# Kernel tuning notes

Measured on AMD Instinct MI355X. Metric: run time of the kernel, lower is better.

Reference implementation:

```python
import jax, jax.numpy as jnp
import numpy as np

N = 8192          # num nodes
T = 8             # num node types (== num_bases, full basis)
H = 4             # attention heads
IN = 64           # in_feat
OUT = 64          # out_feat


def setup_inputs() -> dict:
    key = jax.random.key(0)
    ks = jax.random.split(key, 9)
    return {
        "agg_msg": jax.random.normal(ks[0], (N, H * IN), dtype=jnp.float32),
        "h": jax.random.normal(ks[1], (N, OUT), dtype=jnp.float32),
        "node_type": jax.random.randint(ks[2], (N,), 0, T),
        "W_att": jax.random.normal(ks[3], (T, H * IN, IN), dtype=jnp.float32) * 0.05,
        "b_att": jax.random.normal(ks[4], (T, OUT), dtype=jnp.float32) * 0.05,
        "W_in": jax.random.normal(ks[5], (T, IN, 3 * OUT), dtype=jnp.float32) * 0.05,
        "W_hid": jax.random.normal(ks[6], (T, OUT, 3 * OUT), dtype=jnp.float32) * 0.05,
        "b_in": jax.random.normal(ks[7], (T, 3 * OUT), dtype=jnp.float32) * 0.05,
        "b_hid": jax.random.normal(ks[8], (T, 3 * OUT), dtype=jnp.float32) * 0.05,
    }


def reference(agg_msg, h, node_type, W_att, b_att, W_in, W_hid, b_in, b_hid):
    # activation on aggregated message (F.relu)
    x = jax.nn.relu(agg_msg)                                 # [N, H*IN]
    # --- attention-head aggregation: per-node-type weight gather + bmm ---
    Wa = W_att[node_type]                                    # [N, H*IN, IN]  (irregular gather)
    x = jnp.einsum('nd,ndo->no', x, Wa) + b_att[node_type]   # [N, IN]
    x = jax.nn.relu(x)
    # --- GRU-style gated update with per-node-type weights ---
    gi = jnp.einsum('ni,nio->no', x, W_in[node_type]) + b_in[node_type]    # [N, 3*OUT]
    gh = jnp.einsum('nk,nko->no', h, W_hid[node_type]) + b_hid[node_type]  # [N, 3*OUT]
    i_r, i_z, i_n = jnp.split(gi, 3, axis=-1)
    h_r, h_z, h_n = jnp.split(gh, 3, axis=-1)
    r = jax.nn.sigmoid(i_r + h_r)
    z = jax.nn.sigmoid(i_z + h_z)
    n = jnp.tanh(i_n + r * h_n)
    h_new = (1.0 - z) * n + z * h                            # [N, OUT]
    return h_new
```

## Files before the change

kernel.cpp:

```cpp
#include <hip/hip_runtime.h>

#define N_NODES 8192
#define T_TYPES 8
#define HIN 256
#define OUTF 64
#define G3 192
#define BM 32
#define MAXBLK 264
#define SCAT_BLKS 32

typedef __attribute__((ext_vector_type(8))) __bf16 bf16x8;
typedef __attribute__((ext_vector_type(4))) float f32x4;

#define WS_CURS 0
#define WS_PERM 256
#define WS_WAT  (256 + 262144)
#define WS_WIT  (WS_WAT + 262144)
#define WS_WHT  (WS_WIT + 196608)
#define WS_CNT  (WS_WHT + 196608)

#define L_XS  0
#define L_WAS 16384
#define L_WIS 49152
#define L_WHS 73728
#define L_YS  98304
#define L_HS  102400
#define L_HF  106496
#define L_IDX 114688
#define L_TOT 114816

#define GLD_LDS16(g, l) __builtin_amdgcn_global_load_lds( \
    (const __attribute__((address_space(1))) void*)(g),   \
    (__attribute__((address_space(3))) void*)(l), 16, 0, 0)

__device__ __forceinline__ unsigned short f2bf(float f) {
    unsigned u = __float_as_uint(f);
    return (unsigned short)((u + 0x7FFFu + ((u >> 16) & 1u)) >> 16);
}
__device__ __forceinline__ int pack2bf(float a, float b) {
    return (int)f2bf(a) | ((int)f2bf(b) << 16);
}

__global__ __launch_bounds__(256) void prep_and_count(
    const float* __restrict__ W_att, const float* __restrict__ W_in,
    const float* __restrict__ W_hid, const int* __restrict__ nt,
    int* __restrict__ counts,
    unsigned short* __restrict__ waT, unsigned short* __restrict__ wiT,
    unsigned short* __restrict__ whT)
{
    __shared__ float Lf[64][68];
    __shared__ int hist[8];
    const int tid = threadIdx.x;
    const int b = blockIdx.x;

    if (b >= 80) {
        int j = b - 80;
        if (tid < 8) hist[tid] = 0;
        __syncthreads();
        int t = nt[j * 256 + tid];
        atomicAdd(&hist[t], 1);
        __syncthreads();
        if (tid < 8) counts[j * 8 + tid] = hist[tid];
        return;
    }

    const float* src;
    unsigned short* dstBase;
    int srcStride, rowBytes, colBase, rBase;

    if (b < 32) {
        int t = b >> 2, kt = b & 3;
        src = W_att + (((size_t)t * 256 + kt * 64) << 6);
        srcStride = 64;
        dstBase = waT + (size_t)t * 16384;
        rowBytes = 512; colBase = kt * 128; rBase = 0;
    } else {
        int j = b - 32;
        int isWh = (j >= 24); if (isWh) j -= 24;
        int t = j / 3, nt2 = j - t * 3;
        src = (isWh ? W_hid : W_in) + (size_t)t * 64 * 192 + nt2 * 64;
        srcStride = 192;
        dstBase = (isWh ? whT : wiT) + (size_t)t * 12288;
        rowBytes = 128; colBase = 0; rBase = nt2 * 64;
    }

    #pragma unroll
    for (int e = 0; e < 4; ++e) {
        int f = e * 256 + tid;
        int kk = f >> 4, c = (f & 15) << 2;
        float4 v = *(const float4*)(src + kk * srcStride + c);
        Lf[kk][c] = v.x; Lf[kk][c + 1] = v.y; Lf[kk][c + 2] = v.z; Lf[kk][c + 3] = v.w;
    }
    __syncthreads();

    #pragma unroll
    for (int e = 0; e < 2; ++e) {
        int q = e * 256 + tid;
        int ko8 = q >> 6, rl = q & 63;
        int r = rBase + rl;
        unsigned short tmp[8];
        #pragma unroll
        for (int j2 = 0; j2 < 8; ++j2)
            tmp[j2] = f2bf(Lf[ko8 * 8 + j2][rl]);
        int4 wv;
        wv.x = (int)tmp[0] | ((int)tmp[1] << 16);
        wv.y = (int)tmp[2] | ((int)tmp[3] << 16);
        wv.z = (int)tmp[4] | ((int)tmp[5] << 16);
        wv.w = (int)tmp[6] | ((int)tmp[7] << 16);
        int B = r * rowBytes + colBase + ((ko8 << 4) ^ ((r & 7) << 4));
        *(int4*)((char*)dstBase + B) = wv;
    }
}

__global__ __launch_bounds__(256) void scatter_pass(
    const int* __restrict__ nt, const int* __restrict__ counts,
    int* __restrict__ cursors, int* __restrict__ perm)
{
    __shared__ int tbl[SCAT_BLKS * 8];
    __shared__ int cur[8];
    const int tid = threadIdx.x;
    const int j = blockIdx.x;

    tbl[tid & 255] = counts[tid & 255];
    __syncthreads();
    if (tid < 8) {
        int base = 0, tot = 0;
        #pragma unroll
        for (int b = 0; b < SCAT_BLKS; ++b) {
            int c = tbl[b * 8 + tid];
            if (b < j) base += c;
            tot += c;
        }
        cur[tid] = base;
        if (j == 0) cursors[tid] = tot;
    }
    __syncthreads();
    int i = j * 256 + tid;
    int t = nt[i];
    int pos = atomicAdd(&cur[t], 1);
    perm[t * N_NODES + pos] = i;
}

__global__ __launch_bounds__(256) void fused_rgnn(
    const float* __restrict__ agg, const float* __restrict__ h,
    const int* __restrict__ cursors, const int* __restrict__ perm,
    const unsigned short* __restrict__ waT, const unsigned short* __restrict__ wiT,
    const unsigned short* __restrict__ whT,
    const float* __restrict__ b_att, const float* __restrict__ b_in,
    const float* __restrict__ b_hid, float* __restrict__ out)
{
    __shared__ __align__(16) char smem[L_TOT];
    char* sm = smem;

    const int tid = threadIdx.x;
    const int b = blockIdx.x;

    const int4 c0 = *(const int4*)cursors;
    const int4 c1 = *(const int4*)(cursors + 4);
    const int cntArr[8] = {c0.x, c0.y, c0.z, c0.w, c1.x, c1.y, c1.z, c1.w};
    int t = -1, chunk = 0, cnt = 0, acc = 0;
    #pragma unroll
    for (int tt = 0; tt < T_TYPES; ++tt) {
        int nc = (cntArr[tt] + BM - 1) >> 5;
        if (t < 0 && b < acc + nc) { t = tt; chunk = b - acc; cnt = cntArr[tt]; }
        acc += nc;
    }
    if (t < 0) return;
    const int m0 = chunk * BM;
    const int mcnt = min(BM, cnt - m0);

    const int lane = tid & 63;
    const int w = tid >> 6;
    const int lr = lane & 15;
    const int lk = lane >> 4;
    const int col = (w << 4) + lr;
    const int swzA = (lr & 7) << 4;

    const float ba  = b_att[(t << 6) + col];
    const float bir = b_in [t * G3 + col];
    const float biz = b_in [t * G3 + 64 + col];
    const float bnn = b_in [t * G3 + 128 + col];
    const float bhr = b_hid[t * G3 + col];
    const float bhz = b_hid[t * G3 + 64 + col];
    const float bhn = b_hid[t * G3 + 128 + col];

    const int nb = tid >> 5;
    const int kx = (tid & 31) << 3;
    int xg[4];
    #pragma unroll
    for (int s = 0; s < 4; ++s) {
        int node = nb + (s << 3);
        xg[s] = (node < mcnt) ? perm[t * N_NODES + m0 + node] : -1;
    }
    const int nh = tid >> 3;
    const int kh = (tid & 7) << 3;
    int hg = (nh < mcnt) ? perm[t * N_NODES + m0 + nh] : -1;

    float4 xv[4][2];
    #pragma unroll
    for (int s = 0; s < 4; ++s) {
        if (xg[s] >= 0) {
            const float* p = agg + (size_t)xg[s] * HIN + kx;
            xv[s][0] = *(const float4*)p;
            xv[s][1] = *(const float4*)(p + 4);
        } else {
            xv[s][0] = make_float4(0.f, 0.f, 0.f, 0.f);
            xv[s][1] = make_float4(0.f, 0.f, 0.f, 0.f);
        }
    }
    float4 hv0, hv1;
    if (hg >= 0) {
        const float* p = h + (size_t)hg * OUTF + kh;
        hv0 = *(const float4*)p;
        hv1 = *(const float4*)(p + 4);
    } else {
        hv0 = make_float4(0.f, 0.f, 0.f, 0.f);
        hv1 = make_float4(0.f, 0.f, 0.f, 0.f);
    }

    {
        const char* was = (const char*)(waT + (size_t)t * 16384);
        const char* wis = (const char*)(wiT + (size_t)t * 12288);
        const char* whs = (const char*)(whT + (size_t)t * 12288);
        #pragma unroll
        for (int r = 0; r < 8; ++r) {
            int c = (r << 2) + w;
            GLD_LDS16(was + (c << 10) + (lane << 4), sm + L_WAS + (c << 10));
        }
        #pragma unroll
        for (int r = 0; r < 6; ++r) {
            int c = (r << 2) + w;
            GLD_LDS16(wis + (c << 10) + (lane << 4), sm + L_WIS + (c << 10));
            GLD_LDS16(whs + (c << 10) + (lane << 4), sm + L_WHS + (c << 10));
        }
    }

    #pragma unroll
    for (int s = 0; s < 4; ++s) {
        int node = nb + (s << 3);
        float4 a = xv[s][0], bq = xv[s][1];
        int4 wv;
        wv.x = pack2bf(fmaxf(a.x, 0.f), fmaxf(a.y, 0.f));
        wv.y = pack2bf(fmaxf(a.z, 0.f), fmaxf(a.w, 0.f));
        wv.z = pack2bf(fmaxf(bq.x, 0.f), fmaxf(bq.y, 0.f));
        wv.w = pack2bf(fmaxf(bq.z, 0.f), fmaxf(bq.w, 0.f));
        *(int4*)(sm + L_XS + (node << 9) + (((kx << 1)) ^ ((node & 7) << 4))) = wv;
    }
    {
        *(float4*)(sm + L_HF + (nh << 8) + (kh << 2)) = hv0;
        *(float4*)(sm + L_HF + (nh << 8) + (kh << 2) + 16) = hv1;
        int4 wv;
        wv.x = pack2bf(hv0.x, hv0.y);
        wv.y = pack2bf(hv0.z, hv0.w);
        wv.z = pack2bf(hv1.x, hv1.y);
        wv.w = pack2bf(hv1.z, hv1.w);
        *(int4*)(sm + L_HS + (nh << 7) + ((kh << 1) ^ ((nh & 7) << 4))) = wv;
        if ((tid & 7) == 0) ((int*)(sm + L_IDX))[nh] = hg;
    }
    __syncthreads();

    f32x4 acc0 = {0.f, 0.f, 0.f, 0.f}, acc1 = {0.f, 0.f, 0.f, 0.f};
    #pragma unroll
    for (int ks = 0; ks < 8; ++ks) {
        int koffB = (ks << 6) + (lk << 4);
        int off = koffB ^ swzA;
        bf16x8 bb = *(const bf16x8*)(sm + L_WAS + (((w << 4) + lr) << 9) + off);
        bf16x8 a0 = *(const bf16x8*)(sm + L_XS + (lr << 9) + off);
        bf16x8 a1 = *(const bf16x8*)(sm + L_XS + ((16 + lr) << 9) + off);
        acc0 = __builtin_amdgcn_mfma_f32_16x16x32_bf16(a0, bb, acc0, 0, 0, 0);
        acc1 = __builtin_amdgcn_mfma_f32_16x16x32_bf16(a1, bb, acc1, 0, 0, 0);
    }
    #pragma unroll
    for (int m = 0; m < 2; ++m) {
        #pragma unroll
        for (int r = 0; r < 4; ++r) {
            int row = (m << 4) + (lk << 2) + r;
            float y = fmaxf((m ? acc1[r] : acc0[r]) + ba, 0.f);
            *(unsigned short*)(sm + L_YS + (row << 7) +
                               (((col << 1)) ^ ((row & 7) << 4))) = f2bf(y);
        }
    }
    __syncthreads();

    f32x4 gi[2][3], gh[2][3];
    #pragma unroll
    for (int m = 0; m < 2; ++m)
        #pragma unroll
        for (int g = 0; g < 3; ++g) {
            gi[m][g] = (f32x4){0.f, 0.f, 0.f, 0.f};
            gh[m][g] = (f32x4){0.f, 0.f, 0.f, 0.f};
        }
    #pragma unroll
    for (int ks = 0; ks < 2; ++ks) {
        int off = ((ks << 6) + (lk << 4)) ^ swzA;
        bf16x8 ay0 = *(const bf16x8*)(sm + L_YS + (lr << 7) + off);
        bf16x8 ay1 = *(const bf16x8*)(sm + L_YS + ((16 + lr) << 7) + off);
        bf16x8 ah0 = *(const bf16x8*)(sm + L_HS + (lr << 7) + off);
        bf16x8 ah1 = *(const bf16x8*)(sm + L_HS + ((16 + lr) << 7) + off);
        #pragma unroll
        for (int g = 0; g < 3; ++g) {
            int brow = (g << 6) + col;
            bf16x8 bi = *(const bf16x8*)(sm + L_WIS + (brow << 7) + off);
            bf16x8 bh = *(const bf16x8*)(sm + L_WHS + (brow << 7) + off);
            gi[0][g] = __builtin_amdgcn_mfma_f32_16x16x32_bf16(ay0, bi, gi[0][g], 0, 0, 0);
            gi[1][g] = __builtin_amdgcn_mfma_f32_16x16x32_bf16(ay1, bi, gi[1][g], 0, 0, 0);
            gh[0][g] = __builtin_amdgcn_mfma_f32_16x16x32_bf16(ah0, bh, gh[0][g], 0, 0, 0);
            gh[1][g] = __builtin_amdgcn_mfma_f32_16x16x32_bf16(ah1, bh, gh[1][g], 0, 0, 0);
        }
    }

    const int* idxp = (const int*)(sm + L_IDX);
    #pragma unroll
    for (int m = 0; m < 2; ++m) {
        #pragma unroll
        for (int r = 0; r < 4; ++r) {
            int node = (m << 4) + (lk << 2) + r;
            if (node < mcnt) {
                float rv = gi[m][0][r] + bir + gh[m][0][r] + bhr;
                float rg = 1.f / (1.f + __expf(-rv));
                float zv = gi[m][1][r] + biz + gh[m][1][r] + bhz;
                float zg = 1.f / (1.f + __expf(-zv));
                float ng = tanhf(gi[m][2][r] + bnn + rg * (gh[m][2][r] + bhn));
                float hold = *(const float*)(sm + L_HF + (node << 8) + (col << 2));
                out[(size_t)idxp[node] * OUTF + col] = (1.f - zg) * ng + zg * hold;
            }
        }
    }
}

extern "C" void kernel_launch(void* const* d_in, const int* in_sizes, int n_in,
                              void* d_out, int out_size, void* d_ws, size_t ws_size,
                              hipStream_t stream) {
    const float* agg   = (const float*)d_in[0];
    const float* h     = (const float*)d_in[1];
    const int*   ntype = (const int*)d_in[2];
    const float* W_att = (const float*)d_in[3];
    const float* b_att = (const float*)d_in[4];
    const float* W_in  = (const float*)d_in[5];
    const float* W_hid = (const float*)d_in[6];
    const float* b_in  = (const float*)d_in[7];
    const float* b_hid = (const float*)d_in[8];
    float* out = (float*)d_out;

    char* ws = (char*)d_ws;
    int* cursors = (int*)(ws + WS_CURS);
    int* perm = (int*)(ws + WS_PERM);
    unsigned short* waT = (unsigned short*)(ws + WS_WAT);
    unsigned short* wiT = (unsigned short*)(ws + WS_WIT);
    unsigned short* whT = (unsigned short*)(ws + WS_WHT);
    int* counts = (int*)(ws + WS_CNT);

    prep_and_count<<<112, 256, 0, stream>>>(W_att, W_in, W_hid, ntype, counts, waT, wiT, whT);
    scatter_pass<<<SCAT_BLKS, 256, 0, stream>>>(ntype, counts, cursors, perm);
    fused_rgnn<<<MAXBLK, 256, 0, stream>>>(agg, h, cursors, perm,
        waT, wiT, whT, b_att, b_in, b_hid, out);
}
```

Measured before the change: 24.57 us.

## Merge three kernels into one cooperative kernel with grid syncs

Replaces the prep/count, scatter and fused compute launches with a single cooperative kernel of 256 blocks that uses grid.sync between phases. The compute phase becomes a grid-stride loop over type chunks, since the grid is smaller than the maximum chunk count. This removes two kernel-launch boundaries. In exchange it adds two grid-wide barriers and a cooperative launch, and a few blocks must process two chunks.

```diff
diff --git a/kernel.cpp b/kernel.cpp
--- a/kernel.cpp
+++ b/kernel.cpp
@@ -1,4 +1,7 @@
 #include <hip/hip_runtime.h>
+#include <hip/hip_cooperative_groups.h>
+
+namespace cg = cooperative_groups;
 
 #define N_NODES 8192
 #define T_TYPES 8
@@ -6,8 +9,7 @@
 #define OUTF 64
 #define G3 192
 #define BM 32
-#define MAXBLK 264
-#define SCAT_BLKS 32
+#define GRID 256
 
 typedef __attribute__((ext_vector_type(8))) __bf16 bf16x8;
 typedef __attribute__((ext_vector_type(4))) float f32x4;
@@ -41,288 +43,277 @@
     return (int)f2bf(a) | ((int)f2bf(b) << 16);
 }
 
-__global__ __launch_bounds__(256) void prep_and_count(
-    const float* __restrict__ W_att, const float* __restrict__ W_in,
-    const float* __restrict__ W_hid, const int* __restrict__ nt,
-    int* __restrict__ counts,
+__global__ __launch_bounds__(256) void mono_rgnn(
+    const float* __restrict__ agg, const float* __restrict__ h,
+    const int* __restrict__ nt,
+    const float* __restrict__ W_att, const float* __restrict__ b_att,
+    const float* __restrict__ W_in, const float* __restrict__ W_hid,
+    const float* __restrict__ b_in, const float* __restrict__ b_hid,
+    int* __restrict__ cursors, int* __restrict__ perm, int* __restrict__ counts,
     unsigned short* __restrict__ waT, unsigned short* __restrict__ wiT,
-    unsigned short* __restrict__ whT)
-{
-    __shared__ float Lf[64][68];
-    __shared__ int hist[8];
-    const int tid = threadIdx.x;
-    const int b = blockIdx.x;
-
-    if (b >= 80) {
-        int j = b - 80;
-        if (tid < 8) hist[tid] = 0;
-        __syncthreads();
-        int t = nt[j * 256 + tid];
-        atomicAdd(&hist[t], 1);
-        __syncthreads();
-        if (tid < 8) counts[j * 8 + tid] = hist[tid];
-        return;
-    }
-
-    const float* src;
-    unsigned short* dstBase;
-    int srcStride, rowBytes, colBase, rBase;
-
-    if (b < 32) {
-        int t = b >> 2, kt = b & 3;
-        src = W_att + (((size_t)t * 256 + kt * 64) << 6);
-        srcStride = 64;
-        dstBase = waT + (size_t)t * 16384;
-        rowBytes = 512; colBase = kt * 128; rBase = 0;
-    } else {
-        int j = b - 32;
-        int isWh = (j >= 24); if (isWh) j -= 24;
-        int t = j / 3, nt2 = j - t * 3;
-        src = (isWh ? W_hid : W_in) + (size_t)t * 64 * 192 + nt2 * 64;
-        srcStride = 192;
-        dstBase = (isWh ? whT : wiT) + (size_t)t * 12288;
-        rowBytes = 128; colBase = 0; rBase = nt2 * 64;
-    }
-
-    #pragma unroll
-    for (int e = 0; e < 4; ++e) {
-        int f = e * 256 + tid;
-        int kk = f >> 4, c = (f & 15) << 2;
-        float4 v = *(const float4*)(src + kk * srcStride + c);
-        Lf[kk][c] = v.x; Lf[kk][c + 1] = v.y; Lf[kk][c + 2] = v.z; Lf[kk][c + 3] = v.w;
-    }
-    __syncthreads();
-
-    #pragma unroll
-    for (int e = 0; e < 2; ++e) {
-        int q = e * 256 + tid;
-        int ko8 = q >> 6, rl = q & 63;
-        int r = rBase + rl;
-        unsigned short tmp[8];
-        #pragma unroll
-        for (int j2 = 0; j2 < 8; ++j2)
-            tmp[j2] = f2bf(Lf[ko8 * 8 + j2][rl]);
-        int4 wv;
-        wv.x = (int)tmp[0] | ((int)tmp[1] << 16);
-        wv.y = (int)tmp[2] | ((int)tmp[3] << 16);
-        wv.z = (int)tmp[4] | ((int)tmp[5] << 16);
-        wv.w = (int)tmp[6] | ((int)tmp[7] << 16);
-        int B = r * rowBytes + colBase + ((ko8 << 4) ^ ((r & 7) << 4));
-        *(int4*)((char*)dstBase + B) = wv;
-    }
-}
-
-__global__ __launch_bounds__(256) void scatter_pass(
-    const int* __restrict__ nt, const int* __restrict__ counts,
-    int* __restrict__ cursors, int* __restrict__ perm)
-{
-    __shared__ int tbl[SCAT_BLKS * 8];
-    __shared__ int cur[8];
-    const int tid = threadIdx.x;
-    const int j = blockIdx.x;
-
-    tbl[tid & 255] = counts[tid & 255];
-    __syncthreads();
-    if (tid < 8) {
-        int base = 0, tot = 0;
-        #pragma unroll
-        for (int b = 0; b < SCAT_BLKS; ++b) {
-            int c = tbl[b * 8 + tid];
-            if (b < j) base += c;
-            tot += c;
-        }
-        cur[tid] = base;
-        if (j == 0) cursors[tid] = tot;
-    }
-    __syncthreads();
-    int i = j * 256 + tid;
-    int t = nt[i];
-    int pos = atomicAdd(&cur[t], 1);
-    perm[t * N_NODES + pos] = i;
-}
-
-__global__ __launch_bounds__(256) void fused_rgnn(
-    const float* __restrict__ agg, const float* __restrict__ h,
-    const int* __restrict__ cursors, const int* __restrict__ perm,
-    const unsigned short* __restrict__ waT, const unsigned short* __restrict__ wiT,
-    const unsigned short* __restrict__ whT,
-    const float* __restrict__ b_att, const float* __restrict__ b_in,
-    const float* __restrict__ b_hid, float* __restrict__ out)
+    unsigned short* __restrict__ whT, float* __restrict__ out)
 {
     __shared__ __align__(16) char smem[L_TOT];
     char* sm = smem;
+    cg::grid_group grid = cg::this_grid();
 
     const int tid = threadIdx.x;
     const int b = blockIdx.x;
 
-    const int4 c0 = *(const int4*)cursors;
-    const int4 c1 = *(const int4*)(cursors + 4);
-    const int cntArr[8] = {c0.x, c0.y, c0.z, c0.w, c1.x, c1.y, c1.z, c1.w};
-    int t = -1, chunk = 0, cnt = 0, acc = 0;
-    #pragma unroll
-    for (int tt = 0; tt < T_TYPES; ++tt) {
-        int nc = (cntArr[tt] + BM - 1) >> 5;
-        if (t < 0 && b < acc + nc) { t = tt; chunk = b - acc; cnt = cntArr[tt]; }
-        acc += nc;
+    if (b < 80) {
+        float (*Lf)[68] = (float(*)[68])(sm + L_WAS);
+        const float* src;
+        unsigned short* dstBase;
+        int srcStride, rowBytes, colBase, rBase;
+        if (b < 32) {
+            int t = b >> 2, kt = b & 3;
+            src = W_att + (((size_t)t * 256 + kt * 64) << 6);
+            srcStride = 64;
+            dstBase = waT + (size_t)t * 16384;
+            rowBytes = 512; colBase = kt * 128; rBase = 0;
+        } else {
+            int j = b - 32;
+            int isWh = (j >= 24); if (isWh) j -= 24;
+            int t = j / 3, nt2 = j - t * 3;
+            src = (isWh ? W_hid : W_in) + (size_t)t * 64 * 192 + nt2 * 64;
+            srcStride = 192;
+            dstBase = (isWh ? whT : wiT) + (size_t)t * 12288;
+            rowBytes = 128; colBase = 0; rBase = nt2 * 64;
+        }
+        #pragma unroll
+        for (int e = 0; e < 4; ++e) {
+            int f = e * 256 + tid;
+            int kk = f >> 4, c = (f & 15) << 2;
+            float4 v = *(const float4*)(src + kk * srcStride + c);
+            Lf[kk][c] = v.x; Lf[kk][c + 1] = v.y; Lf[kk][c + 2] = v.z; Lf[kk][c + 3] = v.w;
+        }
+        __syncthreads();
+        #pragma unroll
+        for (int e = 0; e < 2; ++e) {
+            int q = e * 256 + tid;
+            int ko8 = q >> 6, rl = q & 63;
+            int r = rBase + rl;
+            unsigned short tmp[8];
+            #pragma unroll
+            for (int j2 = 0; j2 < 8; ++j2)
+                tmp[j2] = f2bf(Lf[ko8 * 8 + j2][rl]);
+            int4 wv;
+            wv.x = (int)tmp[0] | ((int)tmp[1] << 16);
+            wv.y = (int)tmp[2] | ((int)tmp[3] << 16);
+            wv.z = (int)tmp[4] | ((int)tmp[5] << 16);
+            wv.w = (int)tmp[6] | ((int)tmp[7] << 16);
+            int B = r * rowBytes + colBase + ((ko8 << 4) ^ ((r & 7) << 4));
+            *(int4*)((char*)dstBase + B) = wv;
+        }
+    } else if (b < 112) {
+        int j = b - 80;
+        int* hist = (int*)(sm + L_IDX);
+        if (tid < 8) hist[tid] = 0;
+        __syncthreads();
+        atomicAdd(&hist[nt[j * 256 + tid]], 1);
+        __syncthreads();
+        if (tid < 8) counts[j * 8 + tid] = hist[tid];
     }
-    if (t < 0) return;
-    const int m0 = chunk * BM;
-    const int mcnt = min(BM, cnt - m0);
+
+    grid.sync();
+
+    if (b < 32) {
+        int* tbl = (int*)sm;
+        int* cur = (int*)(sm + 1024);
+        tbl[tid] = counts[tid];
+        __syncthreads();
+        if (tid < 8) {
+            int base = 0, tot = 0;
+            #pragma unroll
+            for (int k = 0; k < 32; ++k) {
+                int c = tbl[k * 8 + tid];
+                if (k < b) base += c;
+                tot += c;
+            }
+            cur[tid] = base;
+            if (b == 0) cursors[tid] = tot;
+        }
+        __syncthreads();
+        int i = b * 256 + tid;
+        int t = nt[i];
+        int pos = atomicAdd(&cur[t], 1);
+        perm[t * N_NODES + pos] = i;
+    }
+
+    grid.sync();
 
     const int lane = tid & 63;
     const int w = tid >> 6;
     const int lr = lane & 15;
     const int lk = lane >> 4;
-    const int col = (w << 4) + lr;
     const int swzA = (lr & 7) << 4;
 
-    const float ba  = b_att[(t << 6) + col];
-    const float bir = b_in [t * G3 + col];
-    const float biz = b_in [t * G3 + 64 + col];
-    const float bnn = b_in [t * G3 + 128 + col];
-    const float bhr = b_hid[t * G3 + col];
-    const float bhz = b_hid[t * G3 + 64 + col];
-    const float bhn = b_hid[t * G3 + 128 + col];
-
-    const int nb = tid >> 5;
-    const int kx = (tid & 31) << 3;
-    int xg[4];
-    #pragma unroll
-    for (int s = 0; s < 4; ++s) {
-        int node = nb + (s << 3);
-        xg[s] = (node < mcnt) ? perm[t * N_NODES + m0 + node] : -1;
-    }
-    const int nh = tid >> 3;
-    const int kh = (tid & 7) << 3;
-    int hg = (nh < mcnt) ? perm[t * N_NODES + m0 + nh] : -1;
-
-    float4 xv[4][2];
-    #pragma unroll
-    for (int s = 0; s < 4; ++s) {
-        if (xg[s] >= 0) {
-            const float* p = agg + (size_t)xg[s] * HIN + kx;
-            xv[s][0] = *(const float4*)p;
-            xv[s][1] = *(const float4*)(p + 4);
+    const int4 c0 = *(const int4*)cursors;
+    const int4 c1 = *(const int4*)(cursors + 4);
+    const int cntArr[8] = {c0.x, c0.y, c0.z, c0.w, c1.x, c1.y, c1.z, c1.w};
+
+    for (int cb = b; ; cb += GRID) {
+        int t = -1, chunk = 0, cnt = 0, acc = 0;
+        #pragma unroll
+        for (int tt = 0; tt < T_TYPES; ++tt) {
+            int nc = (cntArr[tt] + BM - 1) >> 5;
+            if (t < 0 && cb < acc + nc) { t = tt; chunk = cb - acc; cnt = cntArr[tt]; }
+            acc += nc;
+        }
+        if (t < 0) break;
+        const int m0 = chunk * BM;
+        const int mcnt = min(BM, cnt - m0);
+        const int col = (w << 4) + lr;
+
+        __syncthreads();
+
+        const float ba  = b_att[(t << 6) + col];
+        const float bir = b_in [t * G3 + col];
+        const float biz = b_in [t * G3 + 64 + col];
+        const float bnn = b_in [t * G3 + 128 + col];
+        const float bhr = b_hid[t * G3 + col];
+        const float bhz = b_hid[t * G3 + 64 + col];
+        const float bhn = b_hid[t * G3 + 128 + col];
+
+        const int nb = tid >> 5;
+        const int kx = (tid & 31) << 3;
+        int xg[4];
+        #pragma unroll
+        for (int s = 0; s < 4; ++s) {
+            int node = nb + (s << 3);
+            xg[s] = (node < mcnt) ? perm[t * N_NODES + m0 + node] : -1;
+        }
+        const int nh = tid >> 3;
+        const int kh = (tid & 7) << 3;
+        int hg = (nh < mcnt) ? perm[t * N_NODES + m0 + nh] : -1;
+
+        float4 xv[4][2];
+        #pragma unroll
+        for (int s = 0; s < 4; ++s) {
+            if (xg[s] >= 0) {
+                const float* p = agg + (size_t)xg[s] * HIN + kx;
+                xv[s][0] = *(const float4*)p;
+                xv[s][1] = *(const float4*)(p + 4);
+            } else {
+                xv[s][0] = make_float4(0.f, 0.f, 0.f, 0.f);
+                xv[s][1] = make_float4(0.f, 0.f, 0.f, 0.f);
+            }
+        }
+        float4 hv0, hv1;
+        if (hg >= 0) {
+            const float* p = h + (size_t)hg * OUTF + kh;
+            hv0 = *(const float4*)p;
+            hv1 = *(const float4*)(p + 4);
         } else {
-            xv[s][0] = make_float4(0.f, 0.f, 0.f, 0.f);
-            xv[s][1] = make_float4(0.f, 0.f, 0.f, 0.f);
-        }
-    }
-    float4 hv0, hv1;
-    if (hg >= 0) {
-        const float* p = h + (size_t)hg * OUTF + kh;
-        hv0 = *(const float4*)p;
-        hv1 = *(const float4*)(p + 4);
-    } else {
-        hv0 = make_float4(0.f, 0.f, 0.f, 0.f);
-        hv1 = make_float4(0.f, 0.f, 0.f, 0.f);
-    }
-
-    {
-        const char* was = (const char*)(waT + (size_t)t * 16384);
-        const char* wis = (const char*)(wiT + (size_t)t * 12288);
-        const char* whs = (const char*)(whT + (size_t)t * 12288);
-        #pragma unroll
-        for (int r = 0; r < 8; ++r) {
-            int c = (r << 2) + w;
-            GLD_LDS16(was + (c << 10) + (lane << 4), sm + L_WAS + (c << 10));
-        }
-        #pragma unroll
-        for (int r = 0; r < 6; ++r) {
-            int c = (r << 2) + w;
-            GLD_LDS16(wis + (c << 10) + (lane << 4), sm + L_WIS + (c << 10));
-            GLD_LDS16(whs + (c << 10) + (lane << 4), sm + L_WHS + (c << 10));
-        }
-    }
-
-    #pragma unroll
-    for (int s = 0; s < 4; ++s) {
-        int node = nb + (s << 3);
-        float4 a = xv[s][0], bq = xv[s][1];
-        int4 wv;
-        wv.x = pack2bf(fmaxf(a.x, 0.f), fmaxf(a.y, 0.f));
-        wv.y = pack2bf(fmaxf(a.z, 0.f), fmaxf(a.w, 0.f));
-        wv.z = pack2bf(fmaxf(bq.x, 0.f), fmaxf(bq.y, 0.f));
-        wv.w = pack2bf(fmaxf(bq.z, 0.f), fmaxf(bq.w, 0.f));
-        *(int4*)(sm + L_XS + (node << 9) + (((kx << 1)) ^ ((node & 7) << 4))) = wv;
-    }
-    {
-        *(float4*)(sm + L_HF + (nh << 8) + (kh << 2)) = hv0;
-        *(float4*)(sm + L_HF + (nh << 8) + (kh << 2) + 16) = hv1;
-        int4 wv;
-        wv.x = pack2bf(hv0.x, hv0.y);
-        wv.y = pack2bf(hv0.z, hv0.w);
-        wv.z = pack2bf(hv1.x, hv1.y);
-        wv.w = pack2bf(hv1.z, hv1.w);
-        *(int4*)(sm + L_HS + (nh << 7) + ((kh << 1) ^ ((nh & 7) << 4))) = wv;
-        if ((tid & 7) == 0) ((int*)(sm + L_IDX))[nh] = hg;
-    }
-    __syncthreads();
-
-    f32x4 acc0 = {0.f, 0.f, 0.f, 0.f}, acc1 = {0.f, 0.f, 0.f, 0.f};
-    #pragma unroll
-    for (int ks = 0; ks < 8; ++ks) {
-        int koffB = (ks << 6) + (lk << 4);
-        int off = koffB ^ swzA;
-        bf16x8 bb = *(const bf16x8*)(sm + L_WAS + (((w << 4) + lr) << 9) + off);
-        bf16x8 a0 = *(const bf16x8*)(sm + L_XS + (lr << 9) + off);
-        bf16x8 a1 = *(const bf16x8*)(sm + L_XS + ((16 + lr) << 9) + off);
-        acc0 = __builtin_amdgcn_mfma_f32_16x16x32_bf16(a0, bb, acc0, 0, 0, 0);
-        acc1 = __builtin_amdgcn_mfma_f32_16x16x32_bf16(a1, bb, acc1, 0, 0, 0);
-    }
-    #pragma unroll
-    for (int m = 0; m < 2; ++m) {
-        #pragma unroll
-        for (int r = 0; r < 4; ++r) {
-            int row = (m << 4) + (lk << 2) + r;
-            float y = fmaxf((m ? acc1[r] : acc0[r]) + ba, 0.f);
-            *(unsigned short*)(sm + L_YS + (row << 7) +
-                               (((col << 1)) ^ ((row & 7) << 4))) = f2bf(y);
-        }
-    }
-    __syncthreads();
-
-    f32x4 gi[2][3], gh[2][3];
-    #pragma unroll
-    for (int m = 0; m < 2; ++m)
-        #pragma unroll
-        for (int g = 0; g < 3; ++g) {
-            gi[m][g] = (f32x4){0.f, 0.f, 0.f, 0.f};
-            gh[m][g] = (f32x4){0.f, 0.f, 0.f, 0.f};
-        }
-    #pragma unroll
-    for (int ks = 0; ks < 2; ++ks) {
-        int off = ((ks << 6) + (lk << 4)) ^ swzA;
-        bf16x8 ay0 = *(const bf16x8*)(sm + L_YS + (lr << 7) + off);
-        bf16x8 ay1 = *(const bf16x8*)(sm + L_YS + ((16 + lr) << 7) + off);
-        bf16x8 ah0 = *(const bf16x8*)(sm + L_HS + (lr << 7) + off);
-        bf16x8 ah1 = *(const bf16x8*)(sm + L_HS + ((16 + lr) << 7) + off);
-        #pragma unroll
-        for (int g = 0; g < 3; ++g) {
-            int brow = (g << 6) + col;
-            bf16x8 bi = *(const bf16x8*)(sm + L_WIS + (brow << 7) + off);
-            bf16x8 bh = *(const bf16x8*)(sm + L_WHS + (brow << 7) + off);
-            gi[0][g] = __builtin_amdgcn_mfma_f32_16x16x32_bf16(ay0, bi, gi[0][g], 0, 0, 0);
-            gi[1][g] = __builtin_amdgcn_mfma_f32_16x16x32_bf16(ay1, bi, gi[1][g], 0, 0, 0);
-            gh[0][g] = __builtin_amdgcn_mfma_f32_16x16x32_bf16(ah0, bh, gh[0][g], 0, 0, 0);
-            gh[1][g] = __builtin_amdgcn_mfma_f32_16x16x32_bf16(ah1, bh, gh[1][g], 0, 0, 0);
-        }
-    }
-
-    const int* idxp = (const int*)(sm + L_IDX);
-    #pragma unroll
-    for (int m = 0; m < 2; ++m) {
-        #pragma unroll
-        for (int r = 0; r < 4; ++r) {
-            int node = (m << 4) + (lk << 2) + r;
-            if (node < mcnt) {
-                float rv = gi[m][0][r] + bir + gh[m][0][r] + bhr;
-                float rg = 1.f / (1.f + __expf(-rv));
-                float zv = gi[m][1][r] + biz + gh[m][1][r] + bhz;
-                float zg = 1.f / (1.f + __expf(-zv));
-                float ng = tanhf(gi[m][2][r] + bnn + rg * (gh[m][2][r] + bhn));
-                float hold = *(const float*)(sm + L_HF + (node << 8) + (col << 2));
-                out[(size_t)idxp[node] * OUTF + col] = (1.f - zg) * ng + zg * hold;
+            hv0 = make_float4(0.f, 0.f, 0.f, 0.f);
+            hv1 = make_float4(0.f, 0.f, 0.f, 0.f);
+        }
+
+        {
+            const char* was = (const char*)(waT + (size_t)t * 16384);
+            const char* wis = (const char*)(wiT + (size_t)t * 12288);
+            const char* whs = (const char*)(whT + (size_t)t * 12288);
+            #pragma unroll
+            for (int r = 0; r < 8; ++r) {
+                int c = (r << 2) + w;
+                GLD_LDS16(was + (c << 10) + (lane << 4), sm + L_WAS + (c << 10));
+            }
+            #pragma unroll
+            for (int r = 0; r < 6; ++r) {
+                int c = (r << 2) + w;
+                GLD_LDS16(wis + (c << 10) + (lane << 4), sm + L_WIS + (c << 10));
+                GLD_LDS16(whs + (c << 10) + (lane << 4), sm + L_WHS + (c << 10));
+            }
+        }
+
+        #pragma unroll
+        for (int s = 0; s < 4; ++s) {
+            int node = nb + (s << 3);
+            float4 a = xv[s][0], bq = xv[s][1];
+            int4 wv;
+            wv.x = pack2bf(fmaxf(a.x, 0.f), fmaxf(a.y, 0.f));
+            wv.y = pack2bf(fmaxf(a.z, 0.f), fmaxf(a.w, 0.f));
+            wv.z = pack2bf(fmaxf(bq.x, 0.f), fmaxf(bq.y, 0.f));
+            wv.w = pack2bf(fmaxf(bq.z, 0.f), fmaxf(bq.w, 0.f));
+            *(int4*)(sm + L_XS + (node << 9) + ((kx << 1) ^ ((node & 7) << 4))) = wv;
+        }
+        {
+            *(float4*)(sm + L_HF + (nh << 8) + (kh << 2)) = hv0;
+            *(float4*)(sm + L_HF + (nh << 8) + (kh << 2) + 16) = hv1;
+            int4 wv;
+            wv.x = pack2bf(hv0.x, hv0.y);
+            wv.y = pack2bf(hv0.z, hv0.w);
+            wv.z = pack2bf(hv1.x, hv1.y);
+            wv.w = pack2bf(hv1.z, hv1.w);
+            *(int4*)(sm + L_HS + (nh << 7) + ((kh << 1) ^ ((nh & 7) << 4))) = wv;
+            if ((tid & 7) == 0) ((int*)(sm + L_IDX))[nh] = hg;
+        }
+        __syncthreads();
+
+        f32x4 acc0 = {0.f, 0.f, 0.f, 0.f}, acc1 = {0.f, 0.f, 0.f, 0.f};
+        #pragma unroll
+        for (int ks = 0; ks < 8; ++ks) {
+            int off = ((ks << 6) + (lk << 4)) ^ swzA;
+            bf16x8 bb = *(const bf16x8*)(sm + L_WAS + (((w << 4) + lr) << 9) + off);
+            bf16x8 a0 = *(const bf16x8*)(sm + L_XS + (lr << 9) + off);
+            bf16x8 a1 = *(const bf16x8*)(sm + L_XS + ((16 + lr) << 9) + off);
+            acc0 = __builtin_amdgcn_mfma_f32_16x16x32_bf16(a0, bb, acc0, 0, 0, 0);
+            acc1 = __builtin_amdgcn_mfma_f32_16x16x32_bf16(a1, bb, acc1, 0, 0, 0);
+        }
+        #pragma unroll
+        for (int m = 0; m < 2; ++m) {
+            #pragma unroll
+            for (int r = 0; r < 4; ++r) {
+                int row = (m << 4) + (lk << 2) + r;
+                float y = fmaxf((m ? acc1[r] : acc0[r]) + ba, 0.f);
+                *(unsigned short*)(sm + L_YS + (row << 7) +
+                                   ((col << 1) ^ ((row & 7) << 4))) = f2bf(y);
+            }
+        }
+        __syncthreads();
+
+        f32x4 gi[2][3], gh[2][3];
+        #pragma unroll
+        for (int m = 0; m < 2; ++m)
+            #pragma unroll
+            for (int g = 0; g < 3; ++g) {
+                gi[m][g] = (f32x4){0.f, 0.f, 0.f, 0.f};
+                gh[m][g] = (f32x4){0.f, 0.f, 0.f, 0.f};
+            }
+        #pragma unroll
+        for (int ks = 0; ks < 2; ++ks) {
+            int off = ((ks << 6) + (lk << 4)) ^ swzA;
+            bf16x8 ay0 = *(const bf16x8*)(sm + L_YS + (lr << 7) + off);
+            bf16x8 ay1 = *(const bf16x8*)(sm + L_YS + ((16 + lr) << 7) + off);
+            bf16x8 ah0 = *(const bf16x8*)(sm + L_HS + (lr << 7) + off);
+            bf16x8 ah1 = *(const bf16x8*)(sm + L_HS + ((16 + lr) << 7) + off);
+            #pragma unroll
+            for (int g = 0; g < 3; ++g) {
+                int brow = (g << 6) + col;
+                bf16x8 bi = *(const bf16x8*)(sm + L_WIS + (brow << 7) + off);
+                bf16x8 bh = *(const bf16x8*)(sm + L_WHS + (brow << 7) + off);
+                gi[0][g] = __builtin_amdgcn_mfma_f32_16x16x32_bf16(ay0, bi, gi[0][g], 0, 0, 0);
+                gi[1][g] = __builtin_amdgcn_mfma_f32_16x16x32_bf16(ay1, bi, gi[1][g], 0, 0, 0);
+                gh[0][g] = __builtin_amdgcn_mfma_f32_16x16x32_bf16(ah0, bh, gh[0][g], 0, 0, 0);
+                gh[1][g] = __builtin_amdgcn_mfma_f32_16x16x32_bf16(ah1, bh, gh[1][g], 0, 0, 0);
+            }
+        }
+
+        const int* idxp = (const int*)(sm + L_IDX);
+        #pragma unroll
+        for (int m = 0; m < 2; ++m) {
+            #pragma unroll
+            for (int r = 0; r < 4; ++r) {
+                int node = (m << 4) + (lk << 2) + r;
+                if (node < mcnt) {
+                    float rv = gi[m][0][r] + bir + gh[m][0][r] + bhr;
+                    float rg = 1.f / (1.f + __expf(-rv));
+                    float zv = gi[m][1][r] + biz + gh[m][1][r] + bhz;
+                    float zg = 1.f / (1.f + __expf(-zv));
+                    float ng = tanhf(gi[m][2][r] + bnn + rg * (gh[m][2][r] + bhn));
+                    float hold = *(const float*)(sm + L_HF + (node << 8) + (col << 2));
+                    out[(size_t)idxp[node] * OUTF + col] = (1.f - zg) * ng + zg * hold;
+                }
             }
         }
     }
@@ -350,8 +341,13 @@
     unsigned short* whT = (unsigned short*)(ws + WS_WHT);
     int* counts = (int*)(ws + WS_CNT);
 
-    prep_and_count<<<112, 256, 0, stream>>>(W_att, W_in, W_hid, ntype, counts, waT, wiT, whT);
-    scatter_pass<<<SCAT_BLKS, 256, 0, stream>>>(ntype, counts, cursors, perm);
-    fused_rgnn<<<MAXBLK, 256, 0, stream>>>(agg, h, cursors, perm,
-        waT, wiT, whT, b_att, b_in, b_hid, out);
+    void* args[] = {
+        (void*)&agg, (void*)&h, (void*)&ntype,
+        (void*)&W_att, (void*)&b_att, (void*)&W_in, (void*)&W_hid,
+        (void*)&b_in, (void*)&b_hid,
+        (void*)&cursors, (void*)&perm, (void*)&counts,
+        (void*)&waT, (void*)&wiT, (void*)&whT, (void*)&out
+    };
+    hipLaunchCooperativeKernel((const void*)mono_rgnn, dim3(GRID), dim3(256),
+                               args, 0, stream);
 }
```

Result: slower. 84.98 us (+245.8%).

## Fuse histogram and scatter into one block of the prep kernel

Applied to the files above, without the earlier changes.

Merges the separate per-block histogram and scatter kernels into a single block inside the weight-prep kernel. That block counts types per thread over 32 nodes, does a packed 16-bit-lane block scan, and writes the per-type permutation directly. This removes one kernel launch and the global counts round trip. The cost is that one block now serially handles all 8192 nodes with divergent per-element scatter writes, which may become the critical path of the prep kernel.

```diff
diff --git a/kernel.cpp b/kernel.cpp
--- a/kernel.cpp
+++ b/kernel.cpp
@@ -7,7 +7,6 @@
 #define G3 192
 #define BM 32
 #define MAXBLK 264
-#define SCAT_BLKS 32
 
 typedef __attribute__((ext_vector_type(8))) __bf16 bf16x8;
 typedef __attribute__((ext_vector_type(4))) float f32x4;
@@ -17,7 +16,6 @@
 #define WS_WAT  (256 + 262144)
 #define WS_WIT  (WS_WAT + 262144)
 #define WS_WHT  (WS_WIT + 196608)
-#define WS_CNT  (WS_WHT + 196608)
 
 #define L_XS  0
 #define L_WAS 16384
@@ -41,33 +39,87 @@
     return (int)f2bf(a) | ((int)f2bf(b) << 16);
 }
 
-__global__ __launch_bounds__(256) void prep_and_count(
+__global__ __launch_bounds__(256) void prep_and_scatter(
     const float* __restrict__ W_att, const float* __restrict__ W_in,
     const float* __restrict__ W_hid, const int* __restrict__ nt,
-    int* __restrict__ counts,
+    int* __restrict__ cursors, int* __restrict__ perm,
     unsigned short* __restrict__ waT, unsigned short* __restrict__ wiT,
     unsigned short* __restrict__ whT)
 {
     __shared__ float Lf[64][68];
-    __shared__ int hist[8];
+    __shared__ unsigned long long scA[256], scB[256];
     const int tid = threadIdx.x;
     const int b = blockIdx.x;
 
-    if (b >= 80) {
-        int j = b - 80;
-        if (tid < 8) hist[tid] = 0;
+    if (b == 80) {
+        int ty[32];
+        {
+            const int4* p = (const int4*)(nt + tid * 32);
+            #pragma unroll
+            for (int q = 0; q < 8; ++q) {
+                int4 v = p[q];
+                ty[q * 4 + 0] = v.x; ty[q * 4 + 1] = v.y;
+                ty[q * 4 + 2] = v.z; ty[q * 4 + 3] = v.w;
+            }
+        }
+        int cnt[8];
+        #pragma unroll
+        for (int tt = 0; tt < 8; ++tt) cnt[tt] = 0;
+        #pragma unroll
+        for (int k = 0; k < 32; ++k) {
+            int t = ty[k];
+            #pragma unroll
+            for (int tt = 0; tt < 8; ++tt) cnt[tt] += (t == tt);
+        }
+        unsigned long long lo = (unsigned long long)cnt[0]
+                              | ((unsigned long long)cnt[1] << 16)
+                              | ((unsigned long long)cnt[2] << 32)
+                              | ((unsigned long long)cnt[3] << 48);
+        unsigned long long hi = (unsigned long long)cnt[4]
+                              | ((unsigned long long)cnt[5] << 16)
+                              | ((unsigned long long)cnt[6] << 32)
+                              | ((unsigned long long)cnt[7] << 48);
+        scA[tid] = lo; scB[tid] = hi;
+        #pragma unroll
+        for (int ofs = 1; ofs < 256; ofs <<= 1) {
+            __syncthreads();
+            unsigned long long aLo = (tid >= ofs) ? scA[tid - ofs] : 0ull;
+            unsigned long long aHi = (tid >= ofs) ? scB[tid - ofs] : 0ull;
+            __syncthreads();
+            scA[tid] += aLo; scB[tid] += aHi;
+        }
         __syncthreads();
-        int t = nt[j * 256 + tid];
-        atomicAdd(&hist[t], 1);
-        __syncthreads();
-        if (tid < 8) counts[j * 8 + tid] = hist[tid];
+        unsigned long long exLo = scA[tid] - lo, exHi = scB[tid] - hi;
+        if (tid == 255) {
+            unsigned long long tLo = scA[255], tHi = scB[255];
+            #pragma unroll
+            for (int tt = 0; tt < 4; ++tt) {
+                cursors[tt]     = (int)((tLo >> (16 * tt)) & 0xFFFFull);
+                cursors[tt + 4] = (int)((tHi >> (16 * tt)) & 0xFFFFull);
+            }
+        }
+        int P[8], r[8];
+        #pragma unroll
+        for (int tt = 0; tt < 4; ++tt) {
+            P[tt]     = (int)((exLo >> (16 * tt)) & 0xFFFFull);
+            P[tt + 4] = (int)((exHi >> (16 * tt)) & 0xFFFFull);
+        }
+        #pragma unroll
+        for (int tt = 0; tt < 8; ++tt) r[tt] = 0;
+        #pragma unroll
+        for (int k = 0; k < 32; ++k) {
+            int t = ty[k];
+            int i = tid * 32 + k;
+            #pragma unroll
+            for (int tt = 0; tt < 8; ++tt)
+                if (t == tt) { perm[tt * N_NODES + P[tt] + r[tt]] = i; r[tt]++; }
+        }
         return;
     }
 
     const float* src;
     unsigned short* dstBase;
     int srcStride, rowBytes, colBase, rBase;
-
     if (b < 32) {
         int t = b >> 2, kt = b & 3;
         src = W_att + (((size_t)t * 256 + kt * 64) << 6);
@@ -112,35 +164,6 @@
     }
 }
 
-__global__ __launch_bounds__(256) void scatter_pass(
-    const int* __restrict__ nt, const int* __restrict__ counts,
-    int* __restrict__ cursors, int* __restrict__ perm)
-{
-    __shared__ int tbl[SCAT_BLKS * 8];
-    __shared__ int cur[8];
-    const int tid = threadIdx.x;
-    const int j = blockIdx.x;
-
-    tbl[tid & 255] = counts[tid & 255];
-    __syncthreads();
-    if (tid < 8) {
-        int base = 0, tot = 0;
-        #pragma unroll
-        for (int b = 0; b < SCAT_BLKS; ++b) {
-            int c = tbl[b * 8 + tid];
-            if (b < j) base += c;
-            tot += c;
-        }
-        cur[tid] = base;
-        if (j == 0) cursors[tid] = tot;
-    }
-    __syncthreads();
-    int i = j * 256 + tid;
-    int t = nt[i];
-    int pos = atomicAdd(&cur[t], 1);
-    perm[t * N_NODES + pos] = i;
-}
-
 __global__ __launch_bounds__(256) void fused_rgnn(
     const float* __restrict__ agg, const float* __restrict__ h,
     const int* __restrict__ cursors, const int* __restrict__ perm,
@@ -244,7 +267,7 @@
         wv.y = pack2bf(fmaxf(a.z, 0.f), fmaxf(a.w, 0.f));
         wv.z = pack2bf(fmaxf(bq.x, 0.f), fmaxf(bq.y, 0.f));
         wv.w = pack2bf(fmaxf(bq.z, 0.f), fmaxf(bq.w, 0.f));
-        *(int4*)(sm + L_XS + (node << 9) + (((kx << 1)) ^ ((node & 7) << 4))) = wv;
+        *(int4*)(sm + L_XS + (node << 9) + ((kx << 1) ^ ((node & 7) << 4))) = wv;
     }
     {
         *(float4*)(sm + L_HF + (nh << 8) + (kh << 2)) = hv0;
@@ -262,8 +285,7 @@
     f32x4 acc0 = {0.f, 0.f, 0.f, 0.f}, acc1 = {0.f, 0.f, 0.f, 0.f};
     #pragma unroll
     for (int ks = 0; ks < 8; ++ks) {
-        int koffB = (ks << 6) + (lk << 4);
-        int off = koffB ^ swzA;
+        int off = ((ks << 6) + (lk << 4)) ^ swzA;
         bf16x8 bb = *(const bf16x8*)(sm + L_WAS + (((w << 4) + lr) << 9) + off);
         bf16x8 a0 = *(const bf16x8*)(sm + L_XS + (lr << 9) + off);
         bf16x8 a1 = *(const bf16x8*)(sm + L_XS + ((16 + lr) << 9) + off);
@@ -277,7 +299,7 @@
             int row = (m << 4) + (lk << 2) + r;
             float y = fmaxf((m ? acc1[r] : acc0[r]) + ba, 0.f);
             *(unsigned short*)(sm + L_YS + (row << 7) +
-                               (((col << 1)) ^ ((row & 7) << 4))) = f2bf(y);
+                               ((col << 1) ^ ((row & 7) << 4))) = f2bf(y);
         }
     }
     __syncthreads();
@@ -348,10 +370,9 @@
     unsigned short* waT = (unsigned short*)(ws + WS_WAT);
     unsigned short* wiT = (unsigned short*)(ws + WS_WIT);
     unsigned short* whT = (unsigned short*)(ws + WS_WHT);
-    int* counts = (int*)(ws + WS_CNT);
-
-    prep_and_count<<<112, 256, 0, stream>>>(W_att, W_in, W_hid, ntype, counts, waT, wiT, whT);
-    scatter_pass<<<SCAT_BLKS, 256, 0, stream>>>(ntype, counts, cursors, perm);
+
+    prep_and_scatter<<<81, 256, 0, stream>>>(W_att, W_in, W_hid, ntype,
+                                             cursors, perm, waT, wiT, whT);
     fused_rgnn<<<MAXBLK, 256, 0, stream>>>(agg, h, cursors, perm,
         waT, wiT, whT, b_att, b_in, b_hid, out);
 }
```

Measured after the change: 33.01 us. +34.3%, slower.
